# Kernel tuning notes

Measured on AMD Instinct MI355X. Metric: run time of the kernel, lower is better.

Reference implementation:

```python
import jax, jax.numpy as jnp
import numpy as np

K = 3          # kernel_size
PAD = 1        # padding
FOCAL = 50.0
DMIN = 1.0
DMAX = 50.0
ORIG_H = 512.0  # original_image_size[1]


def setup_inputs() -> dict:
    key = jax.random.key(0)
    k1, k2 = jax.random.split(key)
    x = jax.random.normal(k1, (4, 64, 256, 256), dtype=jnp.float32)
    # conv weight [out_ch, in_ch, K, K] (bias=False)
    W = jax.random.normal(k2, (64, 64, K, K), dtype=jnp.float32) * 0.05
    return {"x": x, "W": W}


def _bilinear(img, xs, ys):
    """Bilinear sample img [B,C,H,W] at float pixel coords xs, ys [B,Ho,Wo].
    Zero padding outside the image (grid_sample semantics)."""
    B, C, H, Wd = img.shape
    Ho, Wo = xs.shape[1], xs.shape[2]
    x0 = jnp.floor(xs); y0 = jnp.floor(ys)
    wx1 = xs - x0; wx0 = 1.0 - wx1
    wy1 = ys - y0; wy0 = 1.0 - wy1
    img_flat = img.reshape(B, C, H * Wd)

    def gat(ix, iy):
        ixi = ix.astype(jnp.int32); iyi = iy.astype(jnp.int32)
        valid = (ixi >= 0) & (ixi < Wd) & (iyi >= 0) & (iyi < H)
        idx = jnp.clip(iyi, 0, H - 1) * Wd + jnp.clip(ixi, 0, Wd - 1)
        v = jnp.take_along_axis(img_flat, idx.reshape(B, 1, Ho * Wo), axis=2)
        v = v.reshape(B, C, Ho, Wo)
        return v * valid[:, None].astype(img.dtype)

    return (gat(x0, y0) * (wx0 * wy0)[:, None]
            + gat(x0 + 1, y0) * (wx1 * wy0)[:, None]
            + gat(x0, y0 + 1) * (wx0 * wy1)[:, None]
            + gat(x0 + 1, y0 + 1) * (wx1 * wy1)[:, None])


def reference(x, W):
    B, C, H, Wd = x.shape
    downsample = ORIG_H / H  # 2.0 for H=256

    # upper branch: plain 3x3 conv, padding 1, no bias
    x_upper = jax.lax.conv_general_dilated(x, W, (1, 1), [(PAD, PAD), (PAD, PAD)])

    # geometry -> clamped depth (geometry_method='max', formulation='depth')
    depth = jnp.clip(jnp.max(x, axis=1), DMIN, DMAX)  # [B,H,W]

    # Frontal homography: Hom01 = I with [1,2] = focal/(downsample*depth);
    # its inverse Hom10 shifts y by -s.
    s = FOCAL / (downsample * depth)  # [B,H,W]

    xi = jnp.arange(Wd, dtype=x.dtype)[None, None, :]
    yi = jnp.arange(H, dtype=x.dtype)[None, :, None]
    xs = jnp.broadcast_to(xi, (B, H, Wd))
    ys = yi - s  # Hom10 applied to pixel coords

    # warp input with per-pixel Hom10 (pass_warped_images=True)
    x2 = _bilinear(x, xs, ys)

    # deformable conv: per-pixel offset from Hom10 is (dx,dy)=(0,-s) for all 9 taps
    x_lower = jnp.zeros_like(x_upper)
    for ky in range(K):
        for kx in range(K):
            sx = xs + (kx - PAD)
            sy = ys + (ky - PAD)
            tap = _bilinear(x2, sx, sy)  # [B,C,H,W]
            x_lower = x_lower + jnp.einsum('bchw,oc->bohw', tap, W[:, :, ky, kx])

    # project with 'min' over the stacked (upper, lower) branches
    return jnp.minimum(x_upper, x_lower)
```

## Files before the change

kernel.cpp:

```cpp
#include <hip/hip_runtime.h>
#include <cmath>

constexpr int BB = 4, CC = 64, HH = 256, WW = 256;
constexpr int WP = 258;
constexpr int C2R = 257;

typedef short short8 __attribute__((ext_vector_type(8)));
typedef float f32x4 __attribute__((ext_vector_type(4)));
#define MFMA_BF16 __builtin_amdgcn_mfma_f32_16x16x32_bf16

union U16x8 { uint4 v; unsigned short h[8]; };
union U16x4 { uint2 v; unsigned short h[4]; };

__device__ inline unsigned short f2bf(float f) {
  unsigned u = __builtin_bit_cast(unsigned, f);
  u += 0x7fffu + ((u >> 16) & 1u);
  return (unsigned short)(u >> 16);
}
__device__ inline unsigned short f2bf_trunc(float f) {
  return (unsigned short)(__builtin_bit_cast(unsigned, f) >> 16);
}
__device__ inline float bf2f(unsigned short h) {
  unsigned u = ((unsigned)h) << 16;
  return __builtin_bit_cast(float, u);
}

__global__ __launch_bounds__(256, 4) void k_pack(const float* __restrict__ x,
                                                 float* __restrict__ s,
                                                 unsigned short* __restrict__ xn) {
  __shared__ float tile[CC * 129];
  __shared__ float pmax[2][128];
  const int t = threadIdx.x;
  const int half = blockIdx.x & 1, y = blockIdx.x >> 1, b = blockIdx.y;
  const int px0 = half * 128;
  const int pxl = t & 127, chb = (t >> 7) * 32;

  const float* base = x + (size_t)b * CC * HH * WW + (size_t)y * WW + px0 + pxl;
  float m = -1e30f;
#pragma unroll 8
  for (int i = 0; i < 32; ++i) {
    float v = base[(size_t)(chb + i) * HH * WW];
    tile[(chb + i) * 129 + pxl] = v;
    m = fmaxf(m, v);
  }
  pmax[t >> 7][pxl] = m;

  uint4* xn4 = (uint4*)xn;
  if (t < 8) {
    int col = half ? (WP - 1) : 0;
    xn4[(((size_t)(b * HH + y) * WP + col) * CC + t * 8) >> 3] =
        make_uint4(0, 0, 0, 0);
  }
  __syncthreads();

  if (t < 128) {
    float mm = fmaxf(pmax[0][t], pmax[1][t]);
    s[(b * HH + y) * WW + px0 + t] = 25.0f / fminf(fmaxf(mm, 1.0f), 50.0f);
  }
#pragma unroll
  for (int g = 0; g < 4; ++g) {
    int px = g * 32 + (t >> 3), c8 = t & 7;
    U16x8 r;
#pragma unroll
    for (int j = 0; j < 8; ++j) r.h[j] = f2bf(tile[(c8 * 8 + j) * 129 + px]);
    xn4[(((size_t)(b * HH + y) * WP + px0 + px + 1) * CC + c8 * 8) >> 3] = r.v;
  }
}

__global__ __launch_bounds__(256) void k_wpack(const float* __restrict__ Wt,
                                               unsigned short* __restrict__ Wp) {
  int gid = blockIdx.x * 256 + threadIdx.x;
  int lane = gid & 63, kc = (gid >> 6) & 1, mt = (gid >> 7) & 3, tap = gid >> 9;
  int o = mt * 16 + (lane & 15);
  int kb = kc * 32 + (lane >> 4) * 8;
  int ky = tap / 3, kx = tap % 3;
  U16x8 r;
#pragma unroll
  for (int j = 0; j < 8; ++j)
    r.h[j] = f2bf(Wt[o * 576 + (kb + j) * 9 + ky * 3 + kx]);
  ((uint4*)Wp)[gid] = r.v;
}

__global__ __launch_bounds__(256, 4) void k_lower(const unsigned short* __restrict__ xn,
                                                  const unsigned short* __restrict__ Wp,
                                                  const float* __restrict__ s,
                                                  unsigned short* __restrict__ c2) {
  __shared__ uint4 lds[2112];
  const int t = threadIdx.x;
  const int ctile = blockIdx.x & 3, tr = blockIdx.x >> 2;
  const int b = blockIdx.y;
  const int r0 = tr * 2 - 1;
  const int colBase = ctile * 64;

  const uint4* xn4 = (const uint4*)xn;
#pragma unroll 1
  for (int g = 0; g < 3; ++g) {
    float w0a[3], w1a[3];
    int o0a[3], o1a[3], la[3];
    bool act[3], va[3];
#pragma unroll
    for (int j = 0; j < 3; ++j) {
      int idx = (g * 3 + j) * 256 + t;
      act[j] = idx < 2112;
      int rr_ = idx / 528, rem = idx % 528;
      int col_ = rem >> 3, ch_ = rem & 7;
      int xrow = r0 - 1 + rr_;
      va[j] = act[j] && (xrow >= 0) && (xrow < HH);
      la[j] = (rr_ * 66 + col_) * 8 + (ch_ ^ (col_ & 7));
      float sv = 0.0f;
      int pxc = min(max(colBase + col_ - 1, 0), WW - 1);
      if (va[j]) sv = s[(b * HH + min(max(xrow, 0), HH - 1)) * WW + pxc];
      float ys = (float)xrow - sv;
      float fy = floorf(ys);
      float wfr = ys - fy;
      int i0 = (int)fy;
      w0a[j] = (i0 >= 0) ? 1.0f - wfr : 0.0f;
      w1a[j] = (i0 + 1 >= 0) ? wfr : 0.0f;
      int a0 = min(max(i0, 0), HH - 1), a1 = min(max(i0 + 1, 0), HH - 1);
      o0a[j] = ((b * HH + a0) * WP + colBase + col_) * 8 + ch_;
      o1a[j] = ((b * HH + a1) * WP + colBase + col_) * 8 + ch_;
    }
#pragma unroll
    for (int j = 0; j < 3; ++j) {
      if (act[j]) {
        uint4 v = make_uint4(0, 0, 0, 0);
        if (va[j]) {
          U16x8 u0, u1, rr;
          u0.v = xn4[o0a[j]];
          u1.v = xn4[o1a[j]];
#pragma unroll
          for (int k = 0; k < 8; ++k)
            rr.h[k] = f2bf_trunc(w0a[j] * bf2f(u0.h[k]) + w1a[j] * bf2f(u1.h[k]));
          v = rr.v;
        }
        lds[la[j]] = v;
      }
    }
  }

  const int lane = t & 63, w = t >> 6;
  const int ow = w & 1, ch2 = w >> 1;
  const int quad = lane >> 4, l15 = lane & 15;
  const uint4* wp4 = (const uint4*)Wp;
  __syncthreads();

  f32x4 acc[2][2][2];
#pragma unroll
  for (int pt = 0; pt < 2; ++pt)
#pragma unroll
    for (int rr = 0; rr < 2; ++rr)
#pragma unroll
      for (int ct = 0; ct < 2; ++ct) acc[pt][rr][ct] = {0.f, 0.f, 0.f, 0.f};

#pragma unroll 1
  for (int kc = 0; kc < 2; ++kc) {
    short8 wf[9][2];
#pragma unroll
    for (int tap = 0; tap < 9; ++tap)
#pragma unroll
      for (int ct = 0; ct < 2; ++ct)
        wf[tap][ct] = __builtin_bit_cast(
            short8, wp4[((tap * 4 + (ow * 2 + ct)) * 2 + kc) * 64 + lane]);
#pragma unroll
    for (int pt = 0; pt < 2; ++pt) {
#pragma unroll
      for (int ir = 0; ir < 4; ++ir) {
#pragma unroll
        for (int kx = 0; kx < 3; ++kx) {
          int col = ch2 * 32 + pt * 16 + l15 + kx;
          short8 xf = __builtin_bit_cast(
              short8, lds[(ir * 66 + col) * 8 + ((kc * 4 + quad) ^ (col & 7))]);
          if (ir <= 2) {
#pragma unroll
            for (int ct = 0; ct < 2; ++ct)
              acc[pt][0][ct] = MFMA_BF16(wf[ir * 3 + kx][ct], xf, acc[pt][0][ct], 0, 0, 0);
          }
          if (ir >= 1) {
#pragma unroll
            for (int ct = 0; ct < 2; ++ct)
              acc[pt][1][ct] = MFMA_BF16(wf[(ir - 1) * 3 + kx][ct], xf, acc[pt][1][ct], 0, 0, 0);
          }
        }
      }
    }
  }

  uint2* c2u = (uint2*)c2;
#pragma unroll
  for (int pt = 0; pt < 2; ++pt) {
    int px = colBase + ch2 * 32 + pt * 16 + l15;
#pragma unroll
    for (int rr = 0; rr < 2; ++rr) {
      int r = r0 + rr;
      if (r > 255) continue;
#pragma unroll
      for (int ct = 0; ct < 2; ++ct) {
        f32x4 A = acc[pt][rr][ct];
        int og = (ow * 2 + ct) * 4 + quad;
        unsigned short h0 = f2bf(A[0]), h1 = f2bf(A[1]), h2 = f2bf(A[2]), h3 = f2bf(A[3]);
        uint2 val = make_uint2((unsigned)h0 | ((unsigned)h1 << 16),
                               (unsigned)h2 | ((unsigned)h3 << 16));
        c2u[(size_t)((b * 16 + og) * C2R + (r + 1)) * WW + px] = val;
      }
    }
  }
}

__global__ __launch_bounds__(256, 4) void k_final(const unsigned short* __restrict__ xn,
                                                  const unsigned short* __restrict__ Wp,
                                                  const float* __restrict__ s,
                                                  const unsigned short* __restrict__ c2,
                                                  float* __restrict__ out) {
  __shared__ uint4 lds[2112];
  const int t = threadIdx.x;
  const int ctile = blockIdx.x & 3, tr = blockIdx.x >> 2;
  const int b = blockIdx.y;
  const int y0 = tr * 2;
  const int colBase = ctile * 64;

  const uint4* src4 = (const uint4*)xn;
#pragma unroll 1
  for (int i = 0; i < 9; ++i) {
    int idx = i * 256 + t;
    if (idx < 2112) {
      int rr_ = idx / 528, rem = idx % 528;
      int col_ = rem >> 3, ch_ = rem & 7;
      int xrow = y0 - 1 + rr_;
      uint4 v = make_uint4(0, 0, 0, 0);
      if (xrow >= 0 && xrow < HH)
        v = src4[((size_t)(b * HH + xrow) * WP + colBase + col_) * 8 + ch_];
      lds[(rr_ * 66 + col_) * 8 + (ch_ ^ (col_ & 7))] = v;
    }
  }

  const int lane = t & 63, w = t >> 6;
  const int ow = w & 1, ch2 = w >> 1;
  const int quad = lane >> 4, l15 = lane & 15;
  const uint4* wp4 = (const uint4*)Wp;
  __syncthreads();

  f32x4 acc[2][2][2];
#pragma unroll
  for (int pt = 0; pt < 2; ++pt)
#pragma unroll
    for (int rr = 0; rr < 2; ++rr)
#pragma unroll
      for (int ct = 0; ct < 2; ++ct) acc[pt][rr][ct] = {0.f, 0.f, 0.f, 0.f};

#pragma unroll 1
  for (int kc = 0; kc < 2; ++kc) {
    short8 wf[9][2];
#pragma unroll
    for (int tap = 0; tap < 9; ++tap)
#pragma unroll
      for (int ct = 0; ct < 2; ++ct)
        wf[tap][ct] = __builtin_bit_cast(
            short8, wp4[((tap * 4 + (ow * 2 + ct)) * 2 + kc) * 64 + lane]);
#pragma unroll
    for (int pt = 0; pt < 2; ++pt) {
#pragma unroll
      for (int ir = 0; ir < 4; ++ir) {
#pragma unroll
        for (int kx = 0; kx < 3; ++kx) {
          int col = ch2 * 32 + pt * 16 + l15 + kx;
          short8 xf = __builtin_bit_cast(
              short8, lds[(ir * 66 + col) * 8 + ((kc * 4 + quad) ^ (col & 7))]);
          if (ir <= 2) {
#pragma unroll
            for (int ct = 0; ct < 2; ++ct)
              acc[pt][0][ct] = MFMA_BF16(wf[ir * 3 + kx][ct], xf, acc[pt][0][ct], 0, 0, 0);
          }
          if (ir >= 1) {
#pragma unroll
            for (int ct = 0; ct < 2; ++ct)
              acc[pt][1][ct] = MFMA_BF16(wf[(ir - 1) * 3 + kx][ct], xf, acc[pt][1][ct], 0, 0, 0);
          }
        }
      }
    }
  }

  const uint2* c2u = (const uint2*)c2;
#pragma unroll
  for (int pt = 0; pt < 2; ++pt) {
    int px = colBase + ch2 * 32 + pt * 16 + l15;
#pragma unroll
    for (int rr = 0; rr < 2; ++rr) {
      int y = y0 + rr;
      float sv = s[(b * HH + y) * WW + px];
      float ys = (float)y - sv;
      float fy = floorf(ys);
      float wfr = ys - fy;
      int i0 = (int)fy;
      float lw0 = (i0 + 1 >= 0 && i0 + 1 <= HH) ? 1.0f - wfr : 0.0f;
      float lw1 = (i0 + 2 >= 0 && i0 + 2 <= HH) ? wfr : 0.0f;
      int a0 = min(max(i0 + 1, 0), HH);
      int a1 = min(max(i0 + 2, 0), HH);
#pragma unroll
      for (int ct = 0; ct < 2; ++ct) {
        f32x4 A = acc[pt][rr][ct];
        int og = (ow * 2 + ct) * 4 + quad;
        U16x4 v0, v1;
        v0.v = c2u[(size_t)((b * 16 + og) * C2R + a0) * WW + px];
        v1.v = c2u[(size_t)((b * 16 + og) * C2R + a1) * WW + px];
#pragma unroll
        for (int reg = 0; reg < 4; ++reg) {
          float lower = lw0 * bf2f(v0.h[reg]) + lw1 * bf2f(v1.h[reg]);
          out[((size_t)(b * CC + og * 4 + reg) * HH + y) * WW + px] =
              fminf(A[reg], lower);
        }
      }
    }
  }
}

extern "C" void kernel_launch(void* const* d_in, const int* in_sizes, int n_in,
                              void* d_out, int out_size, void* d_ws, size_t ws_size,
                              hipStream_t stream) {
  const float* x = (const float*)d_in[0];
  const float* Wt = (const float*)d_in[1];
  float* out = (float*)d_out;

  char* ws = (char*)d_ws;
  float* s = (float*)ws;
  unsigned short* Wp = (unsigned short*)(ws + 1048576);
  unsigned short* xn = (unsigned short*)(ws + 1122304);
  unsigned short* c2 = (unsigned short*)(ws + 34938880);
  k_pack<<<dim3(HH * 2, BB), 256, 0, stream>>>(x, s, xn);
  k_wpack<<<dim3(18), 256, 0, stream>>>(Wt, Wp);
  k_lower<<<dim3(4 * 129, BB), 256, 0, stream>>>(xn, Wp, s, c2);
  k_final<<<dim3(4 * 128, BB), 256, 0, stream>>>(xn, Wp, s, c2, out);
}
```

Measured before the change: 189.1 us.

## Stage input channels in two halves to halve LDS and double occupancy

Both conv kernels now load only 32 of the 64 input channels into shared memory per kc iteration, which halves the LDS tile and lets launch bounds rise from 4 to 8 blocks per CU. The swizzle is adapted to the 4-chunk layout, and barriers are added around each half. k_final also prefetches its depth-shift values before the main loop. This trades extra barriers and twice-repeated bilinear index math in k_lower for more resident waves to hide memory latency. The tighter register budget at 8 blocks per CU may cause spills.

```diff
diff --git a/kernel.cpp b/kernel.cpp
--- a/kernel.cpp
+++ b/kernel.cpp
@@ -81,68 +81,22 @@
   ((uint4*)Wp)[gid] = r.v;
 }
 
-__global__ __launch_bounds__(256, 4) void k_lower(const unsigned short* __restrict__ xn,
+__global__ __launch_bounds__(256, 8) void k_lower(const unsigned short* __restrict__ xn,
                                                   const unsigned short* __restrict__ Wp,
                                                   const float* __restrict__ s,
                                                   unsigned short* __restrict__ c2) {
-  __shared__ uint4 lds[2112];
+  __shared__ uint4 lds[1056];
   const int t = threadIdx.x;
   const int ctile = blockIdx.x & 3, tr = blockIdx.x >> 2;
   const int b = blockIdx.y;
   const int r0 = tr * 2 - 1;
   const int colBase = ctile * 64;
 
-  const uint4* xn4 = (const uint4*)xn;
-#pragma unroll 1
-  for (int g = 0; g < 3; ++g) {
-    float w0a[3], w1a[3];
-    int o0a[3], o1a[3], la[3];
-    bool act[3], va[3];
-#pragma unroll
-    for (int j = 0; j < 3; ++j) {
-      int idx = (g * 3 + j) * 256 + t;
-      act[j] = idx < 2112;
-      int rr_ = idx / 528, rem = idx % 528;
-      int col_ = rem >> 3, ch_ = rem & 7;
-      int xrow = r0 - 1 + rr_;
-      va[j] = act[j] && (xrow >= 0) && (xrow < HH);
-      la[j] = (rr_ * 66 + col_) * 8 + (ch_ ^ (col_ & 7));
-      float sv = 0.0f;
-      int pxc = min(max(colBase + col_ - 1, 0), WW - 1);
-      if (va[j]) sv = s[(b * HH + min(max(xrow, 0), HH - 1)) * WW + pxc];
-      float ys = (float)xrow - sv;
-      float fy = floorf(ys);
-      float wfr = ys - fy;
-      int i0 = (int)fy;
-      w0a[j] = (i0 >= 0) ? 1.0f - wfr : 0.0f;
-      w1a[j] = (i0 + 1 >= 0) ? wfr : 0.0f;
-      int a0 = min(max(i0, 0), HH - 1), a1 = min(max(i0 + 1, 0), HH - 1);
-      o0a[j] = ((b * HH + a0) * WP + colBase + col_) * 8 + ch_;
-      o1a[j] = ((b * HH + a1) * WP + colBase + col_) * 8 + ch_;
-    }
-#pragma unroll
-    for (int j = 0; j < 3; ++j) {
-      if (act[j]) {
-        uint4 v = make_uint4(0, 0, 0, 0);
-        if (va[j]) {
-          U16x8 u0, u1, rr;
-          u0.v = xn4[o0a[j]];
-          u1.v = xn4[o1a[j]];
-#pragma unroll
-          for (int k = 0; k < 8; ++k)
-            rr.h[k] = f2bf_trunc(w0a[j] * bf2f(u0.h[k]) + w1a[j] * bf2f(u1.h[k]));
-          v = rr.v;
-        }
-        lds[la[j]] = v;
-      }
-    }
-  }
-
   const int lane = t & 63, w = t >> 6;
   const int ow = w & 1, ch2 = w >> 1;
   const int quad = lane >> 4, l15 = lane & 15;
   const uint4* wp4 = (const uint4*)Wp;
-  __syncthreads();
+  const uint4* xn4 = (const uint4*)xn;
 
   f32x4 acc[2][2][2];
 #pragma unroll
@@ -154,6 +108,55 @@
 
 #pragma unroll 1
   for (int kc = 0; kc < 2; ++kc) {
+#pragma unroll
+    for (int g = 0; g < 2; ++g) {
+      const int nj = g ? 2 : 3;
+      float w0a[3], w1a[3];
+      int o0a[3], o1a[3], la[3];
+      bool act[3], va[3];
+#pragma unroll
+      for (int j = 0; j < 3; ++j) {
+        if (j >= nj) break;
+        int idx = (g * 3 + j) * 256 + t;
+        act[j] = idx < 1056;
+        int rr_ = idx / 264, rem = idx % 264;
+        int col_ = rem >> 2, ch_ = rem & 3;
+        int xrow = r0 - 1 + rr_;
+        va[j] = act[j] && (xrow >= 0) && (xrow < HH);
+        la[j] = (rr_ * 66 + col_) * 4 + (ch_ ^ ((col_ >> 1) & 3));
+        float sv = 0.0f;
+        int pxc = min(max(colBase + col_ - 1, 0), WW - 1);
+        if (va[j]) sv = s[(b * HH + min(max(xrow, 0), HH - 1)) * WW + pxc];
+        float ys = (float)xrow - sv;
+        float fy = floorf(ys);
+        float wfr = ys - fy;
+        int i0 = (int)fy;
+        w0a[j] = (i0 >= 0) ? 1.0f - wfr : 0.0f;
+        w1a[j] = (i0 + 1 >= 0) ? wfr : 0.0f;
+        int a0 = min(max(i0, 0), HH - 1), a1 = min(max(i0 + 1, 0), HH - 1);
+        o0a[j] = ((b * HH + a0) * WP + colBase + col_) * 8 + kc * 4 + ch_;
+        o1a[j] = ((b * HH + a1) * WP + colBase + col_) * 8 + kc * 4 + ch_;
+      }
+#pragma unroll
+      for (int j = 0; j < 3; ++j) {
+        if (j >= nj) break;
+        if (act[j]) {
+          uint4 v = make_uint4(0, 0, 0, 0);
+          if (va[j]) {
+            U16x8 u0, u1, rr;
+            u0.v = xn4[o0a[j]];
+            u1.v = xn4[o1a[j]];
+#pragma unroll
+            for (int k = 0; k < 8; ++k)
+              rr.h[k] = f2bf_trunc(w0a[j] * bf2f(u0.h[k]) + w1a[j] * bf2f(u1.h[k]));
+            v = rr.v;
+          }
+          lds[la[j]] = v;
+        }
+      }
+    }
+    __syncthreads();
+
     short8 wf[9][2];
 #pragma unroll
     for (int tap = 0; tap < 9; ++tap)
@@ -169,7 +172,7 @@
         for (int kx = 0; kx < 3; ++kx) {
           int col = ch2 * 32 + pt * 16 + l15 + kx;
           short8 xf = __builtin_bit_cast(
-              short8, lds[(ir * 66 + col) * 8 + ((kc * 4 + quad) ^ (col & 7))]);
+              short8, lds[(ir * 66 + col) * 4 + (quad ^ ((col >> 1) & 3))]);
           if (ir <= 2) {
 #pragma unroll
             for (int ct = 0; ct < 2; ++ct)
@@ -183,6 +186,7 @@
         }
       }
     }
+    __syncthreads();
   }
 
   uint2* c2u = (uint2*)c2;
@@ -206,38 +210,31 @@
   }
 }
 
-__global__ __launch_bounds__(256, 4) void k_final(const unsigned short* __restrict__ xn,
+__global__ __launch_bounds__(256, 8) void k_final(const unsigned short* __restrict__ xn,
                                                   const unsigned short* __restrict__ Wp,
                                                   const float* __restrict__ s,
                                                   const unsigned short* __restrict__ c2,
                                                   float* __restrict__ out) {
-  __shared__ uint4 lds[2112];
+  __shared__ uint4 lds[1056];
   const int t = threadIdx.x;
   const int ctile = blockIdx.x & 3, tr = blockIdx.x >> 2;
   const int b = blockIdx.y;
   const int y0 = tr * 2;
   const int colBase = ctile * 64;
 
-  const uint4* src4 = (const uint4*)xn;
-#pragma unroll 1
-  for (int i = 0; i < 9; ++i) {
-    int idx = i * 256 + t;
-    if (idx < 2112) {
-      int rr_ = idx / 528, rem = idx % 528;
-      int col_ = rem >> 3, ch_ = rem & 7;
-      int xrow = y0 - 1 + rr_;
-      uint4 v = make_uint4(0, 0, 0, 0);
-      if (xrow >= 0 && xrow < HH)
-        v = src4[((size_t)(b * HH + xrow) * WP + colBase + col_) * 8 + ch_];
-      lds[(rr_ * 66 + col_) * 8 + (ch_ ^ (col_ & 7))] = v;
-    }
-  }
-
   const int lane = t & 63, w = t >> 6;
   const int ow = w & 1, ch2 = w >> 1;
   const int quad = lane >> 4, l15 = lane & 15;
+  const uint4* src4 = (const uint4*)xn;
   const uint4* wp4 = (const uint4*)Wp;
-  __syncthreads();
+
+  float sv_e[2][2];
+#pragma unroll
+  for (int pt = 0; pt < 2; ++pt)
+#pragma unroll
+    for (int rr = 0; rr < 2; ++rr)
+      sv_e[pt][rr] =
+          s[(b * HH + (y0 + rr)) * WW + (colBase + ch2 * 32 + pt * 16 + l15)];
 
   f32x4 acc[2][2][2];
 #pragma unroll
@@ -249,6 +246,21 @@
 
 #pragma unroll 1
   for (int kc = 0; kc < 2; ++kc) {
+#pragma unroll
+    for (int i = 0; i < 5; ++i) {
+      int idx = i * 256 + t;
+      if (idx < 1056) {
+        int rr_ = idx / 264, rem = idx % 264;
+        int col_ = rem >> 2, ch_ = rem & 3;
+        int xrow = y0 - 1 + rr_;
+        uint4 v = make_uint4(0, 0, 0, 0);
+        if (xrow >= 0 && xrow < HH)
+          v = src4[((size_t)(b * HH + xrow) * WP + colBase + col_) * 8 + kc * 4 + ch_];
+        lds[(rr_ * 66 + col_) * 4 + (ch_ ^ ((col_ >> 1) & 3))] = v;
+      }
+    }
+    __syncthreads();
+
     short8 wf[9][2];
 #pragma unroll
     for (int tap = 0; tap < 9; ++tap)
@@ -264,7 +276,7 @@
         for (int kx = 0; kx < 3; ++kx) {
           int col = ch2 * 32 + pt * 16 + l15 + kx;
           short8 xf = __builtin_bit_cast(
-              short8, lds[(ir * 66 + col) * 8 + ((kc * 4 + quad) ^ (col & 7))]);
+              short8, lds[(ir * 66 + col) * 4 + (quad ^ ((col >> 1) & 3))]);
           if (ir <= 2) {
 #pragma unroll
             for (int ct = 0; ct < 2; ++ct)
@@ -278,6 +290,7 @@
         }
       }
     }
+    __syncthreads();
   }
 
   const uint2* c2u = (const uint2*)c2;
@@ -287,7 +300,7 @@
 #pragma unroll
     for (int rr = 0; rr < 2; ++rr) {
       int y = y0 + rr;
-      float sv = s[(b * HH + y) * WW + px];
+      float sv = sv_e[pt][rr];
       float ys = (float)y - sv;
       float fy = floorf(ys);
       float wfr = ys - fy;
```

New measurement: 612.1 us. 224% more time.
